# Performance work log

Measured on AMD Instinct MI355X. Metric: run time of the kernel, lower is better.

## Reference

```python
import jax, jax.numpy as jnp
import numpy as np

B, L, D, H = 2, 2048, 1024, 16
DK = D // H  # head_dim = 64


def setup_inputs() -> dict:
    key = jax.random.key(0)
    ks = jax.random.split(key, 12)
    init = lambda k, shape, fan_in: jax.random.uniform(k, shape, jnp.float32, -1.0, 1.0) / np.sqrt(fan_in)
    inp = {
        "query": jax.random.normal(ks[0], (B, L, D), jnp.float32),
        "key": jax.random.normal(ks[1], (B, L, D), jnp.float32),
        "value": jax.random.normal(ks[2], (B, L, D), jnp.float32),
        # causal mask [B, 1, L, L], True = attend
        "mask": jnp.broadcast_to(jnp.tril(jnp.ones((L, L), bool))[None, None], (B, 1, L, L)),
        "wq": init(ks[3], (D, D), D), "bq": jnp.zeros((D,), jnp.float32),
        "wk": init(ks[4], (D, D), D), "bk": jnp.zeros((D,), jnp.float32),
        "wv": init(ks[5], (D, D), D), "bv": jnp.zeros((D,), jnp.float32),
        "wo": init(ks[6], (D, D), D), "bo": jnp.zeros((D,), jnp.float32),
    }
    return inp


def reference(query, key, value, mask, wq, bq, wk, bk, wv, bv, wo, bo):
    b, l, d = query.shape
    split = lambda x: x.reshape(b, l, H, DK).transpose(0, 2, 1, 3)  # B H L dk
    Q = split(query @ wq + bq)
    K = split(key @ wk + bk)
    V = split(value @ wv + bv)
    scores = jnp.einsum("bhqd,bhkd->bhqk", Q, K) / jnp.sqrt(jnp.float32(DK))
    probs = jax.nn.softmax(scores, axis=-1, where=mask)  # masked-out rows contribute 0
    attn = jnp.einsum("bhqk,bhkd->bhqd", probs, V)
    out = attn.transpose(0, 2, 1, 3).reshape(b, l, d)  # B L D
    return out @ wo + bo
```

## Files before the change

kernel.cpp:

```cpp
#include <hip/hip_runtime.h>
#include <hip/hip_bf16.h>

typedef __bf16 bf16x8 __attribute__((ext_vector_type(8)));
typedef __bf16 bf16x4 __attribute__((ext_vector_type(4)));
typedef float floatx4 __attribute__((ext_vector_type(4)));

constexpr int Bn  = 2;
constexpr int Ln  = 2048;
constexpr int Dn  = 1024;
constexpr int Hn  = 16;
constexpr int DKn = 64;
constexpr int Mn  = Bn * Ln;

__device__ __forceinline__ void gload_lds16(const void* g, void* l) {
  __builtin_amdgcn_global_load_lds(
      (const __attribute__((address_space(1))) void*)g,
      (__attribute__((address_space(3))) void*)l, 16, 0, 0);
}

__global__ __launch_bounds__(256) void prep(
    const float* __restrict__ q, const float* __restrict__ k,
    const float* __restrict__ v,
    const float* __restrict__ wq, const float* __restrict__ wk,
    const float* __restrict__ wv, const float* __restrict__ wo,
    __hip_bfloat16* __restrict__ Abf, __hip_bfloat16* __restrict__ wT)
{
  const int z = blockIdx.z;
  __shared__ __bf16 tile[32][33];
  if (z < 3) {
    const float* src = z == 0 ? q : z == 1 ? k : v;
    __hip_bfloat16* d = Abf + (size_t)z * Mn * Dn;
    const int i = blockIdx.x * 256 + threadIdx.x;
    const float4 a = ((const float4*)src)[i * 2];
    const float4 b = ((const float4*)src)[i * 2 + 1];
    bf16x8 o;
    o[0] = (__bf16)a.x; o[1] = (__bf16)a.y; o[2] = (__bf16)a.z; o[3] = (__bf16)a.w;
    o[4] = (__bf16)b.x; o[5] = (__bf16)b.y; o[6] = (__bf16)b.z; o[7] = (__bf16)b.w;
    ((bf16x8*)d)[i] = o;
  } else {
    if (blockIdx.x >= 1024) return;
    const float* src = z == 3 ? wq : z == 4 ? wk : z == 5 ? wv : wo;
    __hip_bfloat16* dst = wT + (size_t)(z - 3) * Dn * Dn;
    const int bx = blockIdx.x & 31, by = blockIdx.x >> 5;
    const int tx = threadIdx.x & 31, ty = threadIdx.x >> 5;
    const int x = bx * 32 + tx, y = by * 32 + ty;
    for (int i = 0; i < 32; i += 8)
      tile[ty + i][tx] = (__bf16)src[(size_t)(y + i) * Dn + x];
    __syncthreads();
    const int x2 = by * 32 + tx, y2 = bx * 32 + ty;
    for (int i = 0; i < 32; i += 8)
      ((__bf16*)dst)[(size_t)(y2 + i) * Dn + x2] = tile[tx][ty + i];
  }
}

__global__ __launch_bounds__(256) void gemm_qkv(
    const __hip_bfloat16* __restrict__ Abf,
    const __hip_bfloat16* __restrict__ wT,
    const float* __restrict__ bq, const float* __restrict__ bk,
    const float* __restrict__ bv,
    __hip_bfloat16* __restrict__ Qp, __hip_bfloat16* __restrict__ Kp,
    __hip_bfloat16* __restrict__ Vt)
{
  constexpr int BK = 32;
  __shared__ __bf16 As[128][BK];
  __shared__ __bf16 Ws[128][BK];
  const int z = blockIdx.z;
  const __hip_bfloat16* A  = Abf + (size_t)z * Mn * Dn;
  const __hip_bfloat16* WT = wT  + (size_t)z * Dn * Dn;
  const float* bias = z == 0 ? bq : z == 1 ? bk : bv;

  const int m0 = blockIdx.x * 128;
  const int n0 = blockIdx.y * 128;
  const int tid  = threadIdx.x;
  const int lane = tid & 63;
  const int wave = tid >> 6;
  const int quad = lane >> 4;
  const int l16  = lane & 15;
  const int wm = (wave >> 1) * 64;
  const int wn = (wave & 1) * 64;
  const int srow = tid >> 2;
  const int scol = (tid & 3) * 8;

  floatx4 acc[4][4];
  for (int i = 0; i < 4; i++)
    for (int j = 0; j < 4; j++)
      acc[i][j] = (floatx4){0.f, 0.f, 0.f, 0.f};

  for (int k0 = 0; k0 < Dn; k0 += BK) {
    for (int half = 0; half < 2; half++) {
      gload_lds16(&A [(size_t)(m0 + srow + half * 64) * Dn + k0 + scol],
                  &As[srow + half * 64][scol]);
      gload_lds16(&WT[(size_t)(n0 + srow + half * 64) * Dn + k0 + scol],
                  &Ws[srow + half * 64][scol]);
    }
    __syncthreads();
    bf16x8 af[4], wf[4];
    for (int i = 0; i < 4; i++) af[i] = *(const bf16x8*)&As[wm + i * 16 + l16][quad * 8];
    for (int j = 0; j < 4; j++) wf[j] = *(const bf16x8*)&Ws[wn + j * 16 + l16][quad * 8];
    if (z == 2) {
      for (int i = 0; i < 4; i++)
        for (int j = 0; j < 4; j++)
          acc[i][j] = __builtin_amdgcn_mfma_f32_16x16x32_bf16(af[i], wf[j], acc[i][j], 0, 0, 0);
    } else {
      for (int i = 0; i < 4; i++)
        for (int j = 0; j < 4; j++)
          acc[i][j] = __builtin_amdgcn_mfma_f32_16x16x32_bf16(wf[j], af[i], acc[i][j], 0, 0, 0);
    }
    __syncthreads();
  }

  if (z == 2) {
    for (int j = 0; j < 4; j++) {
      const int n = n0 + wn + j * 16 + l16;
      const float bvv = bias[n];
      const int h = n >> 6, dk = n & 63;
      for (int i = 0; i < 4; i++) {
        const int m = m0 + wm + i * 16 + quad * 4;
        const int b = m >> 11, li = m & (Ln - 1);
        bf16x4 pk;
        for (int r = 0; r < 4; r++) pk[r] = (__bf16)(acc[i][j][r] + bvv);
        *(bf16x4*)&Vt[(((size_t)(b * Hn + h)) * DKn + dk) * Ln + li] = pk;
      }
    }
  } else {
    __hip_bfloat16* out = z == 0 ? Qp : Kp;
    for (int j = 0; j < 4; j++) {
      const int nq = n0 + wn + j * 16 + quad * 4;
      const float4 b4 = *(const float4*)&bias[nq];
      const int h = nq >> 6, dk = nq & 63;
      for (int i = 0; i < 4; i++) {
        const int m = m0 + wm + i * 16 + l16;
        const int b = m >> 11, li = m & (Ln - 1);
        bf16x4 pk;
        pk[0] = (__bf16)(acc[i][j][0] + b4.x);
        pk[1] = (__bf16)(acc[i][j][1] + b4.y);
        pk[2] = (__bf16)(acc[i][j][2] + b4.z);
        pk[3] = (__bf16)(acc[i][j][3] + b4.w);
        *(bf16x4*)&out[(((size_t)(b * Hn + h)) * Ln + li) * DKn + dk] = pk;
      }
    }
  }
}

__global__ __launch_bounds__(256) void gemm_out(
    const __hip_bfloat16* __restrict__ A,
    const __hip_bfloat16* __restrict__ WT,
    const float* __restrict__ bias,
    float* __restrict__ out)
{
  constexpr int BK = 32;
  __shared__ __bf16 As[128][BK];
  __shared__ __bf16 Ws[64][BK];
  const int m0 = blockIdx.x * 128;
  const int n0 = blockIdx.y * 64;
  const int tid  = threadIdx.x;
  const int lane = tid & 63;
  const int wave = tid >> 6;
  const int quad = lane >> 4;
  const int l16  = lane & 15;
  const int wm = (wave >> 1) * 64;
  const int wn = (wave & 1) * 32;
  const int srow = tid >> 2;
  const int scol = (tid & 3) * 8;

  floatx4 acc[4][2];
  for (int i = 0; i < 4; i++)
    for (int j = 0; j < 2; j++)
      acc[i][j] = (floatx4){0.f, 0.f, 0.f, 0.f};

  for (int k0 = 0; k0 < Dn; k0 += BK) {
    for (int half = 0; half < 2; half++)
      gload_lds16(&A [(size_t)(m0 + srow + half * 64) * Dn + k0 + scol],
                  &As[srow + half * 64][scol]);
    gload_lds16(&WT[(size_t)(n0 + srow) * Dn + k0 + scol], &Ws[srow][scol]);
    __syncthreads();
    bf16x8 af[4], wf[2];
    for (int i = 0; i < 4; i++) af[i] = *(const bf16x8*)&As[wm + i * 16 + l16][quad * 8];
    for (int j = 0; j < 2; j++) wf[j] = *(const bf16x8*)&Ws[wn + j * 16 + l16][quad * 8];
    for (int i = 0; i < 4; i++)
      for (int j = 0; j < 2; j++)
        acc[i][j] = __builtin_amdgcn_mfma_f32_16x16x32_bf16(af[i], wf[j], acc[i][j], 0, 0, 0);
    __syncthreads();
  }

  for (int j = 0; j < 2; j++) {
    const int n = n0 + wn + j * 16 + l16;
    const float bvv = bias[n];
    for (int i = 0; i < 4; i++)
      for (int r = 0; r < 4; r++) {
        const int m = m0 + wm + i * 16 + quad * 4 + r;
        out[(size_t)m * Dn + n] = acc[i][j][r] + bvv;
      }
  }
}

__global__ __launch_bounds__(128) void attn_flash(
    const __hip_bfloat16* __restrict__ Qp,
    const __hip_bfloat16* __restrict__ Kp,
    const __hip_bfloat16* __restrict__ Vt,
    __hip_bfloat16* __restrict__ attn)
{
  const int bh   = blockIdx.x;
  const int pA   = blockIdx.y;
  const int tid  = threadIdx.x;
  const int wave = tid >> 6;
  const int lane = tid & 63;
  const int quad = lane >> 4;
  const int l16  = lane & 15;

  const __hip_bfloat16* Qh = Qp + (size_t)bh * Ln * DKn;
  const __hip_bfloat16* Kh = Kp + (size_t)bh * Ln * DKn;
  const __hip_bfloat16* Vh = Vt + (size_t)bh * DKn * Ln;

  __shared__ __align__(16) __bf16 Ks[2][64][64];
  __shared__ __align__(16) __bf16 Vs[2][64][64];
  __shared__ __align__(16) __bf16 Plds[2][2][16][72];

  const int srow8 = lane >> 3;
  const int gch   = (lane & 7) ^ srow8;
  const int xs    = l16 & 7;
  const int b = bh >> 4, h = bh & 15;

  auto stage = [&](int sbuf, int kt) {
    for (int s = 0; s < 4; s++) {
      const int u = wave * 4 + s;
      gload_lds16(Kh + (size_t)(kt + u * 8 + srow8) * DKn + gch * 8,
                  &Ks[sbuf][u * 8][0] + (size_t)lane * 8);
      gload_lds16(Vh + (size_t)(u * 8 + srow8) * Ln + kt + gch * 8,
                  &Vs[sbuf][u * 8][0] + (size_t)lane * 8);
    }
  };

  for (int half = 0; half < 2; half++) {
    const int qt = half ? 31 - pA : pA;
    const int qw = qt * 64 + wave * 32;

    bf16x8 qf[2][2];
    for (int m = 0; m < 2; m++)
      for (int dd = 0; dd < 2; dd++)
        qf[m][dd] = *(const bf16x8*)&Qh[(size_t)(qw + m * 16 + l16) * DKn + dd * 32 + quad * 8];

    floatx4 o[2][4];
    for (int m = 0; m < 2; m++)
      for (int t = 0; t < 4; t++) o[m][t] = (floatx4){0.f, 0.f, 0.f, 0.f};
    float lp[2] = {0.f, 0.f};

    __syncthreads();
    stage(0, 0);
    int buf = 0;
    const int iters = qt + 1;
    for (int it = 0; it < iters; it++, buf ^= 1) {
      const int kt = it * 64;
      __syncthreads();
      if (it + 1 < iters) stage(buf ^ 1, kt + 64);

      floatx4 s[2][4];
      for (int m = 0; m < 2; m++)
        for (int sub = 0; sub < 4; sub++) s[m][sub] = (floatx4){0.f, 0.f, 0.f, 0.f};
      for (int sub = 0; sub < 4; sub++)
        for (int dd = 0; dd < 2; dd++) {
          bf16x8 kf = *(const bf16x8*)&Ks[buf][sub * 16 + l16][((dd * 4 + quad) ^ xs) * 8];
          s[0][sub] = __builtin_amdgcn_mfma_f32_16x16x32_bf16(kf, qf[0][dd], s[0][sub], 0, 0, 0);
          s[1][sub] = __builtin_amdgcn_mfma_f32_16x16x32_bf16(kf, qf[1][dd], s[1][sub], 0, 0, 0);
        }
      bf16x8 vf[4][2];
      for (int t = 0; t < 4; t++)
        for (int kc = 0; kc < 2; kc++)
          vf[t][kc] = *(const bf16x8*)&Vs[buf][t * 16 + l16][((kc * 4 + quad) ^ xs) * 8];

      for (int m = 0; m < 2; m++) {
        const bool needmask = (kt + 64 > qw + m * 16);
        const int qg = qw + m * 16 + l16;
        for (int sub = 0; sub < 4; sub++) {
          bf16x4 pk;
          for (int r = 0; r < 4; r++) {
            float sv = s[m][sub][r];
            if (needmask && (kt + sub * 16 + quad * 4 + r > qg)) sv = -1e30f;
            const float e = __builtin_exp2f(__builtin_fmaf(sv, 0.18033688f, -11.5415603f));
            lp[m] += e;
            pk[r] = (__bf16)e;
          }
          *(bf16x4*)&Plds[wave][m][l16][sub * 16 + quad * 4] = pk;
        }
      }
      __asm__ volatile("s_waitcnt lgkmcnt(0)" ::: "memory");

      bf16x8 pf[2][2];
      for (int m = 0; m < 2; m++)
        for (int kc = 0; kc < 2; kc++)
          pf[m][kc] = *(const bf16x8*)&Plds[wave][m][l16][kc * 32 + quad * 8];
      for (int m = 0; m < 2; m++)
        for (int t = 0; t < 4; t++)
          for (int kc = 0; kc < 2; kc++)
            o[m][t] = __builtin_amdgcn_mfma_f32_16x16x32_bf16(vf[t][kc], pf[m][kc], o[m][t], 0, 0, 0);
    }

    for (int m = 0; m < 2; m++) {
      float lf = lp[m];
      lf += __shfl_xor(lf, 16);
      lf += __shfl_xor(lf, 32);
      const float inv = 1.0f / lf;
      const int ql = qw + m * 16 + l16;
      const size_t base = ((size_t)b * Ln + ql) * Dn + h * DKn;
      for (int t = 0; t < 4; t++) {
        bf16x4 pk;
        for (int r = 0; r < 4; r++) pk[r] = (__bf16)(o[m][t][r] * inv);
        *(bf16x4*)&attn[base + t * 16 + quad * 4] = pk;
      }
    }
  }
}

extern "C" void kernel_launch(void* const* d_in, const int* in_sizes, int n_in,
                              void* d_out, int out_size, void* d_ws, size_t ws_size,
                              hipStream_t stream) {
  const float* query = (const float*)d_in[0];
  const float* key_  = (const float*)d_in[1];
  const float* value = (const float*)d_in[2];
  const float* wq = (const float*)d_in[4];
  const float* bq = (const float*)d_in[5];
  const float* wk = (const float*)d_in[6];
  const float* bk = (const float*)d_in[7];
  const float* wv = (const float*)d_in[8];
  const float* bv = (const float*)d_in[9];
  const float* wo = (const float*)d_in[10];
  const float* bo = (const float*)d_in[11];

  const size_t T   = (size_t)Mn * Dn;
  const size_t WSZ = (size_t)Dn * Dn;
  __hip_bfloat16* Abf  = (__hip_bfloat16*)d_ws;
  __hip_bfloat16* Qp   = Abf + 3 * T;
  __hip_bfloat16* Kp   = Qp + T;
  __hip_bfloat16* Vt   = Kp + T;
  __hip_bfloat16* wT   = Vt + T;
  __hip_bfloat16* attn = Abf;

  prep<<<dim3(2048, 1, 7), 256, 0, stream>>>(query, key_, value, wq, wk, wv, wo, Abf, wT);
  gemm_qkv<<<dim3(Mn / 128, Dn / 128, 3), 256, 0, stream>>>(Abf, wT, bq, bk, bv, Qp, Kp, Vt);
  attn_flash<<<dim3(Bn * Hn, Ln / 128), 128, 0, stream>>>(Qp, Kp, Vt, attn);
  gemm_out<<<dim3(Mn / 128, Dn / 64), 256, 0, stream>>>(attn, wT + 3 * WSZ, bo, (float*)d_out);
}
```

Baseline: 283.1 us.

## Launch one causal query tile per block with single-buffered LDS and heavy-first order

```diff
diff --git a/kernel.cpp b/kernel.cpp
--- a/kernel.cpp
+++ b/kernel.cpp
@@ -201,19 +201,20 @@
     __hip_bfloat16* __restrict__ attn)
 {
   const int bh   = blockIdx.x;
-  const int pA   = blockIdx.y;
+  const int qt   = gridDim.y - 1 - blockIdx.y;
   const int tid  = threadIdx.x;
   const int wave = tid >> 6;
   const int lane = tid & 63;
   const int quad = lane >> 4;
   const int l16  = lane & 15;
+  const int qw   = qt * 64 + wave * 32;
 
   const __hip_bfloat16* Qh = Qp + (size_t)bh * Ln * DKn;
   const __hip_bfloat16* Kh = Kp + (size_t)bh * Ln * DKn;
   const __hip_bfloat16* Vh = Vt + (size_t)bh * DKn * Ln;
 
-  __shared__ __align__(16) __bf16 Ks[2][64][64];
-  __shared__ __align__(16) __bf16 Vs[2][64][64];
+  __shared__ __align__(16) __bf16 Ks[64][64];
+  __shared__ __align__(16) __bf16 Vs[64][64];
   __shared__ __align__(16) __bf16 Plds[2][2][16][72];
 
   const int srow8 = lane >> 3;
@@ -221,92 +222,90 @@
   const int xs    = l16 & 7;
   const int b = bh >> 4, h = bh & 15;
 
-  auto stage = [&](int sbuf, int kt) {
+  auto stage = [&](int kt) {
     for (int s = 0; s < 4; s++) {
       const int u = wave * 4 + s;
       gload_lds16(Kh + (size_t)(kt + u * 8 + srow8) * DKn + gch * 8,
-                  &Ks[sbuf][u * 8][0] + (size_t)lane * 8);
+                  &Ks[u * 8][0] + (size_t)lane * 8);
       gload_lds16(Vh + (size_t)(u * 8 + srow8) * Ln + kt + gch * 8,
-                  &Vs[sbuf][u * 8][0] + (size_t)lane * 8);
+                  &Vs[u * 8][0] + (size_t)lane * 8);
     }
   };
 
-  for (int half = 0; half < 2; half++) {
-    const int qt = half ? 31 - pA : pA;
-    const int qw = qt * 64 + wave * 32;
-
-    bf16x8 qf[2][2];
+  bf16x8 qf[2][2];
+  for (int m = 0; m < 2; m++)
+    for (int dd = 0; dd < 2; dd++)
+      qf[m][dd] = *(const bf16x8*)&Qh[(size_t)(qw + m * 16 + l16) * DKn + dd * 32 + quad * 8];
+
+  floatx4 o[2][4];
+  for (int m = 0; m < 2; m++)
+    for (int t = 0; t < 4; t++) o[m][t] = (floatx4){0.f, 0.f, 0.f, 0.f};
+  float lp[2] = {0.f, 0.f};
+
+  stage(0);
+  const int iters = qt + 1;
+  for (int it = 0; it < iters; it++) {
+    const int kt = it * 64;
+    __syncthreads();
+
+    bf16x8 kf[4][2], vf[4][2];
+    for (int sub = 0; sub < 4; sub++)
+      for (int dd = 0; dd < 2; dd++)
+        kf[sub][dd] = *(const bf16x8*)&Ks[sub * 16 + l16][((dd * 4 + quad) ^ xs) * 8];
+    for (int t = 0; t < 4; t++)
+      for (int kc = 0; kc < 2; kc++)
+        vf[t][kc] = *(const bf16x8*)&Vs[t * 16 + l16][((kc * 4 + quad) ^ xs) * 8];
+
+    __syncthreads();
+    if (it + 1 < iters) stage(kt + 64);
+
+    floatx4 s[2][4];
     for (int m = 0; m < 2; m++)
-      for (int dd = 0; dd < 2; dd++)
-        qf[m][dd] = *(const bf16x8*)&Qh[(size_t)(qw + m * 16 + l16) * DKn + dd * 32 + quad * 8];
-
-    floatx4 o[2][4];
+      for (int sub = 0; sub < 4; sub++) s[m][sub] = (floatx4){0.f, 0.f, 0.f, 0.f};
+    for (int sub = 0; sub < 4; sub++)
+      for (int dd = 0; dd < 2; dd++) {
+        s[0][sub] = __builtin_amdgcn_mfma_f32_16x16x32_bf16(kf[sub][dd], qf[0][dd], s[0][sub], 0, 0, 0);
+        s[1][sub] = __builtin_amdgcn_mfma_f32_16x16x32_bf16(kf[sub][dd], qf[1][dd], s[1][sub], 0, 0, 0);
+      }
+
+    for (int m = 0; m < 2; m++) {
+      const bool needmask = (kt + 64 > qw + m * 16);
+      const int qg = qw + m * 16 + l16;
+      for (int sub = 0; sub < 4; sub++) {
+        bf16x4 pk;
+        for (int r = 0; r < 4; r++) {
+          float sv = s[m][sub][r];
+          if (needmask && (kt + sub * 16 + quad * 4 + r > qg)) sv = -1e30f;
+          const float e = __builtin_exp2f(__builtin_fmaf(sv, 0.18033688f, -11.5415603f));
+          lp[m] += e;
+          pk[r] = (__bf16)e;
+        }
+        *(bf16x4*)&Plds[wave][m][l16][sub * 16 + quad * 4] = pk;
+      }
+    }
+    __asm__ volatile("s_waitcnt lgkmcnt(0)" ::: "memory");
+
+    bf16x8 pf[2][2];
     for (int m = 0; m < 2; m++)
-      for (int t = 0; t < 4; t++) o[m][t] = (floatx4){0.f, 0.f, 0.f, 0.f};
-    float lp[2] = {0.f, 0.f};
-
-    __syncthreads();
-    stage(0, 0);
-    int buf = 0;
-    const int iters = qt + 1;
-    for (int it = 0; it < iters; it++, buf ^= 1) {
-      const int kt = it * 64;
-      __syncthreads();
-      if (it + 1 < iters) stage(buf ^ 1, kt + 64);
-
-      floatx4 s[2][4];
-      for (int m = 0; m < 2; m++)
-        for (int sub = 0; sub < 4; sub++) s[m][sub] = (floatx4){0.f, 0.f, 0.f, 0.f};
-      for (int sub = 0; sub < 4; sub++)
-        for (int dd = 0; dd < 2; dd++) {
-          bf16x8 kf = *(const bf16x8*)&Ks[buf][sub * 16 + l16][((dd * 4 + quad) ^ xs) * 8];
-          s[0][sub] = __builtin_amdgcn_mfma_f32_16x16x32_bf16(kf, qf[0][dd], s[0][sub], 0, 0, 0);
-          s[1][sub] = __builtin_amdgcn_mfma_f32_16x16x32_bf16(kf, qf[1][dd], s[1][sub], 0, 0, 0);
-        }
-      bf16x8 vf[4][2];
+      for (int kc = 0; kc < 2; kc++)
+        pf[m][kc] = *(const bf16x8*)&Plds[wave][m][l16][kc * 32 + quad * 8];
+    for (int m = 0; m < 2; m++)
       for (int t = 0; t < 4; t++)
         for (int kc = 0; kc < 2; kc++)
-          vf[t][kc] = *(const bf16x8*)&Vs[buf][t * 16 + l16][((kc * 4 + quad) ^ xs) * 8];
-
-      for (int m = 0; m < 2; m++) {
-        const bool needmask = (kt + 64 > qw + m * 16);
-        const int qg = qw + m * 16 + l16;
-        for (int sub = 0; sub < 4; sub++) {
-          bf16x4 pk;
-          for (int r = 0; r < 4; r++) {
-            float sv = s[m][sub][r];
-            if (needmask && (kt + sub * 16 + quad * 4 + r > qg)) sv = -1e30f;
-            const float e = __builtin_exp2f(__builtin_fmaf(sv, 0.18033688f, -11.5415603f));
-            lp[m] += e;
-            pk[r] = (__bf16)e;
-          }
-          *(bf16x4*)&Plds[wave][m][l16][sub * 16 + quad * 4] = pk;
-        }
-      }
-      __asm__ volatile("s_waitcnt lgkmcnt(0)" ::: "memory");
-
-      bf16x8 pf[2][2];
-      for (int m = 0; m < 2; m++)
-        for (int kc = 0; kc < 2; kc++)
-          pf[m][kc] = *(const bf16x8*)&Plds[wave][m][l16][kc * 32 + quad * 8];
-      for (int m = 0; m < 2; m++)
-        for (int t = 0; t < 4; t++)
-          for (int kc = 0; kc < 2; kc++)
-            o[m][t] = __builtin_amdgcn_mfma_f32_16x16x32_bf16(vf[t][kc], pf[m][kc], o[m][t], 0, 0, 0);
-    }
-
-    for (int m = 0; m < 2; m++) {
-      float lf = lp[m];
-      lf += __shfl_xor(lf, 16);
-      lf += __shfl_xor(lf, 32);
-      const float inv = 1.0f / lf;
-      const int ql = qw + m * 16 + l16;
-      const size_t base = ((size_t)b * Ln + ql) * Dn + h * DKn;
-      for (int t = 0; t < 4; t++) {
-        bf16x4 pk;
-        for (int r = 0; r < 4; r++) pk[r] = (__bf16)(o[m][t][r] * inv);
-        *(bf16x4*)&attn[base + t * 16 + quad * 4] = pk;
-      }
+          o[m][t] = __builtin_amdgcn_mfma_f32_16x16x32_bf16(vf[t][kc], pf[m][kc], o[m][t], 0, 0, 0);
+  }
+
+  for (int m = 0; m < 2; m++) {
+    float lf = lp[m];
+    lf += __shfl_xor(lf, 16);
+    lf += __shfl_xor(lf, 32);
+    const float inv = 1.0f / lf;
+    const int ql = qw + m * 16 + l16;
+    const size_t base = ((size_t)b * Ln + ql) * Dn + h * DKn;
+    for (int t = 0; t < 4; t++) {
+      bf16x4 pk;
+      for (int r = 0; r < 4; r++) pk[r] = (__bf16)(o[m][t][r] * inv);
+      *(bf16x4*)&attn[base + t * 16 + quad * 4] = pk;
     }
   }
 }
@@ -337,6 +336,6 @@
 
   prep<<<dim3(2048, 1, 7), 256, 0, stream>>>(query, key_, value, wq, wk, wv, wo, Abf, wT);
   gemm_qkv<<<dim3(Mn / 128, Dn / 128, 3), 256, 0, stream>>>(Abf, wT, bq, bk, bv, Qp, Kp, Vt);
-  attn_flash<<<dim3(Bn * Hn, Ln / 128), 128, 0, stream>>>(Qp, Kp, Vt, attn);
+  attn_flash<<<dim3(Bn * Hn, Ln / 64), 128, 0, stream>>>(Qp, Kp, Vt, attn);
   gemm_out<<<dim3(Mn / 128, Dn / 64), 256, 0, stream>>>(attn, wT + 3 * WSZ, bo, (float*)d_out);
 }
```

Result: faster. 263.3 us (-7.0%).
